# Optimization experiments

Measured on AMD Instinct MI355X. Metric: run time of the kernel, lower is better.

The kernel has to match this reference:

```python
import jax, jax.numpy as jnp
import numpy as np

B, N, D = 64, 128, 32
P = N * (N - 1)          # ordered pairs
H1, H2, HF = 32, 32, 16  # layer_widths=(32,32), final_widths=(16,)
EPS = 1e-5
SLOPE = 0.01             # LeakyReLU default


def _leaky(x):
    return jnp.where(x >= 0, x, SLOPE * x)


def setup_inputs() -> dict:
    key = jax.random.key(0)
    ks = jax.random.split(key, 16)
    # all ordered pairs (i, j), i != j, grouped by source i
    src = np.repeat(np.arange(N), N - 1)
    tgt = np.array([j for i in range(N) for j in range(N) if j != i])
    s = 0.1
    return {
        "inputs": jax.random.normal(ks[0], (B, N, D), jnp.float32),
        "src": jnp.asarray(src, jnp.int32),
        "tgt": jnp.asarray(tgt, jnp.int32),
        # edge MLP: Linear(2D,32) -> BN1d(P) -> LeakyReLU -> Linear(32,32) -> LeakyReLU -> Linear(32, 1+D)
        "W1": jax.random.normal(ks[1], (2 * D, H1), jnp.float32) * s,
        "b1": jnp.zeros((H1,), jnp.float32),
        "g1": jnp.ones((P,), jnp.float32),
        "be1": jnp.zeros((P,), jnp.float32),
        "W2": jax.random.normal(ks[2], (H1, H2), jnp.float32) * s,
        "b2": jnp.zeros((H2,), jnp.float32),
        "W3": jax.random.normal(ks[3], (H2, 1 + D), jnp.float32) * s,
        "b3": jnp.zeros((1 + D,), jnp.float32),
        # final MLP: Linear(2D,16) -> BN1d(16) -> LeakyReLU -> Linear(16, D)
        "Wf1": jax.random.normal(ks[4], (2 * D, HF), jnp.float32) * s,
        "bf1": jnp.zeros((HF,), jnp.float32),
        "gf": jnp.ones((HF,), jnp.float32),
        "bef": jnp.zeros((HF,), jnp.float32),
        "Wf2": jax.random.normal(ks[5], (HF, D), jnp.float32) * s,
        "bf2": jnp.zeros((D,), jnp.float32),
    }


def reference(inputs, src, tgt, W1, b1, g1, be1, W2, b2, W3, b3,
              Wf1, bf1, gf, bef, Wf2, bf2):
    b, n, d = inputs.shape
    # gather pair features: (B, P, 2D)
    paired = jnp.concatenate([inputs[:, src], inputs[:, tgt]], axis=2)
    h = paired @ W1 + b1                              # (B, P, H1)
    # BatchNorm1d(P) on (B, P, H1): normalize per pair channel over (batch, feat)
    m = h.mean(axis=(0, 2), keepdims=True)
    v = h.var(axis=(0, 2), keepdims=True)
    h = (h - m) * jax.lax.rsqrt(v + EPS) * g1[None, :, None] + be1[None, :, None]
    h = _leaky(h) @ W2 + b2
    h = _leaky(h) @ W3 + b3                           # (B, P, 1+D)
    edges = jax.nn.sigmoid(h[..., :1])                # (B, P, 1)
    messages = h[..., 1:]                             # (B, P, D)
    weighted = edges * messages
    # segment-sum over the (N-1) senders per source node
    agg = weighted.reshape(b, n, n - 1, d).sum(axis=2)  # (B, N, D)
    sm = jnp.concatenate([inputs, agg], axis=2).reshape(-1, 2 * d)
    f = sm @ Wf1 + bf1                                # (B*N, HF)
    mf = f.mean(axis=0)
    vf = f.var(axis=0)
    f = (f - mf) * jax.lax.rsqrt(vf + EPS) * gf + bef
    out = _leaky(f) @ Wf2 + bf2
    return edges[..., 0], out.reshape(b, n, d)
```

## Files before the change

### kernel.cpp

```cpp
#include <hip/hip_runtime.h>
#include <hip/hip_bf16.h>
#include <math.h>

#define BB 64
#define NN 128
#define DD 32
#define PP (NN * (NN - 1))
#define EPSF 1e-5f

typedef __attribute__((ext_vector_type(8))) short bf16x8;
typedef __attribute__((ext_vector_type(4))) float f32x4;

static __device__ __forceinline__ unsigned short f2bf(float x) {
    unsigned u = __builtin_bit_cast(unsigned, x);
    u += 0x7fff + ((u >> 16) & 1);
    return (unsigned short)(u >> 16);
}
static __device__ __forceinline__ unsigned pk2bf(float a, float b) {
    float2 t; t.x = a; t.y = b;
    __hip_bfloat162 h = __float22bfloat162_rn(t);
    unsigned u;
    __builtin_memcpy(&u, &h, 4);
    return u;
}
static __device__ __forceinline__ float leakyf(float x) {
    return fmaxf(x, 0.01f * x);
}

__global__ __launch_bounds__(256) void proj_kernel(
    const float* __restrict__ inputs, const float* __restrict__ W1,
    const float* __restrict__ b1,
    const float* __restrict__ W2, const float* __restrict__ W3,
    float* __restrict__ AT, float* __restrict__ BT,
    unsigned short* __restrict__ ATh, unsigned short* __restrict__ BTh,
    float* __restrict__ SQp,
    unsigned short* __restrict__ W2p, unsigned short* __restrict__ W3p,
    float* __restrict__ fpartA, float* __restrict__ fpartB)
{
    __shared__ float Xs[16 * 33];
    __shared__ float W1s[2048];
    __shared__ float red[16];

    int tid = threadIdx.x;
    int n = blockIdx.x >> 2, q = blockIdx.x & 3;

    for (int idx = tid; idx < 2048; idx += 256) W1s[idx] = W1[idx];
    for (int idx = tid; idx < 512; idx += 256) {
        int r = idx >> 5, d = idx & 31;
        Xs[r * 33 + d] = inputs[(size_t)(q * 16 + r) * 4096 + n * 32 + d];
    }
    __syncthreads();

    int j = tid & 31, rb = tid >> 5;
    int lane = tid & 63, w = tid >> 6;
    float b1j = b1[j];
    float sa = 0.f, qa = 0.f, sb = 0.f, qb = 0.f;
    #pragma unroll
    for (int i = 0; i < 2; ++i) {
        int r = rb * 2 + i;
        int b = q * 16 + r;
        float a = b1j, c = 0.f;
        #pragma unroll
        for (int k = 0; k < 32; ++k) {
            float x = Xs[r * 33 + k];
            a += x * W1s[k * 32 + j];
            c += x * W1s[(32 + k) * 32 + j];
        }
        size_t off = ((size_t)n * 64 + b) * 32 + j;
        AT[off] = a;  BT[off] = c;
        ATh[off] = f2bf(a);  BTh[off] = f2bf(c);
        sa += a; qa += a * a; sb += c; qb += c * c;
    }
    #pragma unroll
    for (int d = 32; d > 0; d >>= 1) {
        sa += __shfl_down(sa, d, 64);
        qa += __shfl_down(qa, d, 64);
        sb += __shfl_down(sb, d, 64);
        qb += __shfl_down(qb, d, 64);
    }
    if (lane == 0) { red[w*4+0] = sa; red[w*4+1] = qa; red[w*4+2] = sb; red[w*4+3] = qb; }
    __syncthreads();
    if (tid == 0) {
        float4 v;
        v.x = red[0] + red[4] + red[8]  + red[12];
        v.y = red[1] + red[5] + red[9]  + red[13];
        v.z = red[2] + red[6] + red[10] + red[14];
        v.w = red[3] + red[7] + red[11] + red[15];
        ((float4*)SQp)[n * 4 + q] = v;
    }

    if (blockIdx.x == 0 && tid < 64) {
        int l = tid, nn2 = l & 15, kc = l >> 4;
        #pragma unroll
        for (int ct = 0; ct < 2; ++ct)
            #pragma unroll
            for (int jj = 0; jj < 8; ++jj) {
                int k = kc * 8 + jj;
                W2p[(ct * 64 + l) * 8 + jj] = f2bf(W2[k * 32 + ct * 16 + nn2]);
            }
        #pragma unroll
        for (int ct = 0; ct < 3; ++ct)
            #pragma unroll
            for (int jj = 0; jj < 8; ++jj) {
                int k = kc * 8 + jj;
                int c2 = ct * 16 + nn2;
                W3p[(ct * 64 + l) * 8 + jj] = f2bf(c2 < 33 ? W3[k * 33 + c2] : 0.f);
            }
    }
    if (blockIdx.x == 1) {
        for (int idx = tid; idx < 1024; idx += 256) {
            fpartA[idx] = 0.f;
            fpartB[idx] = 0.f;
        }
    }
}

__global__ __launch_bounds__(256) void stats2_kernel(
    const unsigned short* __restrict__ ATh, const unsigned short* __restrict__ BTh,
    const float* __restrict__ SQp,
    const float* __restrict__ g1, const float* __restrict__ be1,
    float* __restrict__ statA, float* __restrict__ statB)
{
    __shared__ __align__(16) float part[4 * 64 * 4];
    int tid = threadIdx.x;
    int lane = tid & 63, w = tid >> 6;
    int s0 = (blockIdx.x >> 3) * 16, t0 = (blockIdx.x & 7) * 16;

    int m = lane & 15, kc = lane >> 4;
    const unsigned short* abase = ATh + (size_t)(s0 + m) * 2048 + kc * 8 + w * 512;
    const unsigned short* bbase = BTh + (size_t)(t0 + m) * 2048 + kc * 8 + w * 512;

    f32x4 acc0 = {0.f, 0.f, 0.f, 0.f}, acc1 = {0.f, 0.f, 0.f, 0.f};
    #pragma unroll
    for (int step = 0; step < 8; ++step) {
        bf16x8 av0 = *(const bf16x8*)(abase + (2 * step) * 32);
        bf16x8 bv0 = *(const bf16x8*)(bbase + (2 * step) * 32);
        acc0 = __builtin_amdgcn_mfma_f32_16x16x32_bf16(av0, bv0, acc0, 0, 0, 0);
        bf16x8 av1 = *(const bf16x8*)(abase + (2 * step + 1) * 32);
        bf16x8 bv1 = *(const bf16x8*)(bbase + (2 * step + 1) * 32);
        acc1 = __builtin_amdgcn_mfma_f32_16x16x32_bf16(av1, bv1, acc1, 0, 0, 0);
    }
    f32x4 acc;
    acc[0] = acc0[0] + acc1[0]; acc[1] = acc0[1] + acc1[1];
    acc[2] = acc0[2] + acc1[2]; acc[3] = acc0[3] + acc1[3];
    *(f32x4*)&part[(w * 64 + lane) * 4] = acc;
    __syncthreads();

    if (w == 0) {
        #pragma unroll
        for (int ww = 1; ww < 4; ++ww) {
            f32x4 o2 = *(const f32x4*)&part[(ww * 64 + lane) * 4];
            acc[0] += o2[0]; acc[1] += o2[1]; acc[2] += o2[2]; acc[3] += o2[3];
        }
        int col = lane & 15, quad = lane >> 4;
        int t = t0 + col;
        float sbt = 0.f, qbt = 0.f;
        #pragma unroll
        for (int o2 = 0; o2 < 4; ++o2) {
            float4 v = ((const float4*)SQp)[t * 4 + o2];
            sbt += v.z; qbt += v.w;
        }
        #pragma unroll
        for (int r = 0; r < 4; ++r) {
            int s = s0 + quad * 4 + r;
            if (s != t) {
                float sas = 0.f, qas = 0.f;
                #pragma unroll
                for (int o2 = 0; o2 < 4; ++o2) {
                    float4 v = ((const float4*)SQp)[s * 4 + o2];
                    sas += v.x; qas += v.y;
                }
                int e = t - (t > s);
                int p = s * 127 + e;
                float S = sas + sbt;
                float Q = qas + qbt + 2.f * acc[r];
                float mean = S * (1.f / 2048.f);
                float var  = Q * (1.f / 2048.f) - mean * mean;
                float inv  = rsqrtf(var + EPSF);
                float sc   = inv * g1[p];
                statA[p] = sc;
                statB[p] = be1[p] - mean * sc;
            }
        }
    }
}

__global__ __launch_bounds__(256) void edges_kernel(
    const float* __restrict__ AT, const float* __restrict__ BT,
    const float* __restrict__ statA, const float* __restrict__ statB,
    const unsigned short* __restrict__ W2p, const unsigned short* __restrict__ W3p,
    const float* __restrict__ b2, const float* __restrict__ b3,
    const float* __restrict__ inputs, const float* __restrict__ Wf1,
    const float* __restrict__ bf1,
    float* __restrict__ edges_out,
    float* __restrict__ f, float* __restrict__ fpartA, float* __restrict__ fpartB)
{
    __shared__ __align__(16) unsigned short Hs[4][512];
    __shared__ float Wf1s[1024];
    __shared__ float aggbuf[4][32];

    int tid = threadIdx.x;
    int s = blockIdx.x & 127;
    int b = blockIdx.x >> 7;
    int lane = tid & 63, w = tid >> 6;
    int m = lane & 15;
    int kb = lane >> 4;
    int col = m;
    int q4 = kb * 4;
    int qbase = lane & 48;

    for (int idx = tid; idx < 1024; idx += 256) Wf1s[idx] = Wf1[idx];

    bf16x8 wb2[2], wb3[3];
    wb2[0] = *(const bf16x8*)(W2p + (0 * 64 + lane) * 8);
    wb2[1] = *(const bf16x8*)(W2p + (1 * 64 + lane) * 8);
    wb3[0] = *(const bf16x8*)(W3p + (0 * 64 + lane) * 8);
    wb3[1] = *(const bf16x8*)(W3p + (1 * 64 + lane) * 8);
    wb3[2] = *(const bf16x8*)(W3p + (2 * 64 + lane) * 8);
    float b2c0 = b2[col], b2c1 = b2[16 + col];
    float b3c[3];
    #pragma unroll
    for (int ct = 0; ct < 3; ++ct) {
        int c = ct * 16 + col;
        b3c[ct] = (c < 33) ? b3[c] : 0.f;
    }

    const float4* asl = (const float4*)(AT + ((size_t)s * 64 + b) * 32 + kb * 8);
    float4 a0 = asl[0], a1 = asl[1];

    float aggpart[3] = {0.f, 0.f, 0.f};

    #pragma unroll
    for (int rt = 0; rt < 2; ++rt) {
        int tile = w * 2 + rt;
        int e = tile * 16 + m;
        bool valid = (e < 127);
        int ee = valid ? e : 0;
        int t = ee + (ee >= s);
        int p = s * 127 + ee;
        float sc = statA[p], sh = statB[p];

        const float4* bsl = (const float4*)(BT + ((size_t)t * 64 + b) * 32 + kb * 8);
        float4 bv0 = bsl[0], bv1 = bsl[1];

        float nh[8];
        nh[0] = leakyf((a0.x + bv0.x) * sc + sh);
        nh[1] = leakyf((a0.y + bv0.y) * sc + sh);
        nh[2] = leakyf((a0.z + bv0.z) * sc + sh);
        nh[3] = leakyf((a0.w + bv0.w) * sc + sh);
        nh[4] = leakyf((a1.x + bv1.x) * sc + sh);
        nh[5] = leakyf((a1.y + bv1.y) * sc + sh);
        nh[6] = leakyf((a1.z + bv1.z) * sc + sh);
        nh[7] = leakyf((a1.w + bv1.w) * sc + sh);
        if (!valid) {
            #pragma unroll
            for (int q = 0; q < 8; ++q) nh[q] = 0.f;
        }
        union { bf16x8 v; unsigned u[4]; } AF;
        #pragma unroll
        for (int q = 0; q < 4; ++q) AF.u[q] = pk2bf(nh[2*q], nh[2*q+1]);

        f32x4 c0 = {0.f, 0.f, 0.f, 0.f}, c1 = {0.f, 0.f, 0.f, 0.f};
        c0 = __builtin_amdgcn_mfma_f32_16x16x32_bf16(AF.v, wb2[0], c0, 0, 0, 0);
        c1 = __builtin_amdgcn_mfma_f32_16x16x32_bf16(AF.v, wb2[1], c1, 0, 0, 0);

        #pragma unroll
        for (int reg = 0; reg < 4; ++reg) {
            int row = q4 + reg;
            float x = leakyf(c0[reg] + b2c0);
            float y = leakyf(c1[reg] + b2c1);
            int cA = col;
            int cB = col + 16;
            Hs[w][row * 32 + (((cA >> 3) ^ (row >> 2)) & 3) * 8 + (cA & 7)] = f2bf(x);
            Hs[w][row * 32 + (((cB >> 3) ^ (row >> 2)) & 3) * 8 + (cB & 7)] = f2bf(y);
        }
        bf16x8 a2 = *(const bf16x8*)&Hs[w][m * 32 + ((kb ^ (m >> 2)) & 3) * 8];

        f32x4 oo[3];
        #pragma unroll
        for (int ct = 0; ct < 3; ++ct) {
            f32x4 cc = {0.f, 0.f, 0.f, 0.f};
            oo[ct] = __builtin_amdgcn_mfma_f32_16x16x32_bf16(a2, wb3[ct], cc, 0, 0, 0);
        }

        float v0 = 0.f, v1 = 0.f, v2 = 0.f, v3 = 0.f;
        int grow0 = tile * 16 + q4;
        if (col == 0) {
            v0 = 1.f / (1.f + __expf(-(oo[0][0] + b3c[0])));
            v1 = 1.f / (1.f + __expf(-(oo[0][1] + b3c[0])));
            v2 = 1.f / (1.f + __expf(-(oo[0][2] + b3c[0])));
            v3 = (grow0 == 124) ? 0.f
               : 1.f / (1.f + __expf(-(oo[0][3] + b3c[0])));
            float* ep = edges_out + (size_t)b * PP + s * 127 + grow0;
            ep[0] = v0; ep[1] = v1; ep[2] = v2;
            if (grow0 != 124) ep[3] = v3;
        }
        float ev0 = __shfl(v0, qbase, 64);
        float ev1 = __shfl(v1, qbase, 64);
        float ev2 = __shfl(v2, qbase, 64);
        float ev3 = __shfl(v3, qbase, 64);

        #pragma unroll
        for (int ct = 0; ct < 3; ++ct) {
            float bb3 = b3c[ct];
            float pt = ev0 * (oo[ct][0] + bb3) + ev1 * (oo[ct][1] + bb3)
                     + ev2 * (oo[ct][2] + bb3) + ev3 * (oo[ct][3] + bb3);
            aggpart[ct] += pt;
        }
    }

    #pragma unroll
    for (int ct = 0; ct < 3; ++ct) {
        float pt = aggpart[ct];
        pt += __shfl_xor(pt, 16, 64);
        pt += __shfl_xor(pt, 32, 64);
        int c = ct * 16 + col;
        if (kb == 0 && c >= 1 && c <= 32) aggbuf[w][c - 1] = pt;
    }
    __syncthreads();

    if (tid < 16) {
        size_t row = (size_t)b * 128 + s;
        const float* xrow = inputs + row * 32;
        float acc = bf1[tid];
        #pragma unroll
        for (int k = 0; k < 32; ++k) acc += xrow[k] * Wf1s[k * 16 + tid];
        #pragma unroll
        for (int k = 0; k < 32; ++k) {
            float tot = aggbuf[0][k] + aggbuf[1][k] + aggbuf[2][k] + aggbuf[3][k];
            acc += tot * Wf1s[(32 + k) * 16 + tid];
        }
        f[row * 16 + tid] = acc;
        int bucket = blockIdx.x & 63;
        atomicAdd(&fpartA[bucket * 16 + tid], acc);
        atomicAdd(&fpartB[bucket * 16 + tid], acc * acc);
    }
}

__global__ __launch_bounds__(256) void out_kernel(
    const float* __restrict__ f,
    const float* __restrict__ fpartA, const float* __restrict__ fpartB,
    const float* __restrict__ gf, const float* __restrict__ bef,
    const float* __restrict__ Wf2, const float* __restrict__ bf2,
    float* __restrict__ outp)
{
    __shared__ float Wf2s[512];
    __shared__ float sc[16], sh[16];
    __shared__ float fs[128];

    int tid = threadIdx.x;
    for (int idx = tid; idx < 512; idx += 256) Wf2s[idx] = Wf2[idx];
    if (tid < 16) {
        float S = 0.f, Q = 0.f;
        #pragma unroll
        for (int g = 0; g < 64; ++g) {
            S += fpartA[g * 16 + tid];
            Q += fpartB[g * 16 + tid];
        }
        float mean = S * (1.f / 8192.f);
        float var  = Q * (1.f / 8192.f) - mean * mean;
        float inv  = rsqrtf(var + EPSF);
        float s2   = inv * gf[tid];
        sc[tid] = s2;
        sh[tid] = bef[tid] - mean * s2;
    }
    int row0 = blockIdx.x * 8;
    if (tid < 128) {
        int r = tid >> 4, j = tid & 15;
        fs[r * 16 + j] = f[(size_t)(row0 + r) * 16 + j];
    }
    __syncthreads();

    int rl = tid >> 5, d = tid & 31;
    float acc = bf2[d];
    #pragma unroll
    for (int j = 0; j < 16; ++j) {
        float v = fs[rl * 16 + j] * sc[j] + sh[j];
        v = leakyf(v);
        acc += v * Wf2s[j * 32 + d];
    }
    outp[(size_t)(row0 + rl) * 32 + d] = acc;
}

extern "C" void kernel_launch(void* const* d_in, const int* in_sizes, int n_in,
                              void* d_out, int out_size, void* d_ws, size_t ws_size,
                              hipStream_t stream) {
    const float* inputs = (const float*)d_in[0];
    const float* W1   = (const float*)d_in[3];
    const float* b1   = (const float*)d_in[4];
    const float* g1   = (const float*)d_in[5];
    const float* be1  = (const float*)d_in[6];
    const float* W2   = (const float*)d_in[7];
    const float* b2   = (const float*)d_in[8];
    const float* W3   = (const float*)d_in[9];
    const float* b3   = (const float*)d_in[10];
    const float* Wf1  = (const float*)d_in[11];
    const float* bf1  = (const float*)d_in[12];
    const float* gf   = (const float*)d_in[13];
    const float* bef  = (const float*)d_in[14];
    const float* Wf2  = (const float*)d_in[15];
    const float* bf2  = (const float*)d_in[16];

    float* ws = (float*)d_ws;
    float* AT     = ws;
    float* BT     = ws + 262144;
    unsigned short* ATh = (unsigned short*)(ws + 524288);
    unsigned short* BTh = ATh + 262144;
    float* SQp    = ws + 786432;
    float* statA  = ws + 790528;
    float* statB  = ws + 806784;
    float* f      = ws + 823040;
    float* fpartA = ws + 954112;
    float* fpartB = ws + 955136;
    unsigned short* W2p = (unsigned short*)(ws + 956160);
    unsigned short* W3p = W2p + 1024;

    float* edges_out = (float*)d_out;
    float* outp      = edges_out + (size_t)BB * PP;

    proj_kernel<<<512, 256, 0, stream>>>(inputs, W1, b1, W2, W3,
                                         AT, BT, ATh, BTh, SQp,
                                         W2p, W3p, fpartA, fpartB);
    stats2_kernel<<<64, 256, 0, stream>>>(ATh, BTh, SQp, g1, be1, statA, statB);
    edges_kernel<<<8192, 256, 0, stream>>>(AT, BT, statA, statB, W2p, W3p,
                                           b2, b3, inputs, Wf1, bf1,
                                           edges_out, f, fpartA, fpartB);
    out_kernel<<<1024, 256, 0, stream>>>(f, fpartA, fpartB, gf, bef, Wf2, bf2, outp);
}
```

Measured before the change: 144.2 us.

## Fuse four kernels into one persistent kernel with software grid barriers

Merges the projection, pair-statistics, edge MLP and output kernels into a single 1024-block persistent kernel. Atomic-counter grid barriers separate the phases, and the edge phase loops over multiple (batch, source) work items per block. This removes three kernel launch gaps and tail effects, at the cost of spin-wait barriers that need every block co-resident, plus an extra memset launch. Occupancy is capped by a launch bound of 4 blocks per SM.

```diff
diff --git a/kernel.cpp b/kernel.cpp
--- a/kernel.cpp
+++ b/kernel.cpp
@@ -7,6 +7,7 @@
 #define DD 32
 #define PP (NN * (NN - 1))
 #define EPSF 1e-5f
+#define GRID 1024
 
 typedef __attribute__((ext_vector_type(8))) short bf16x8;
 typedef __attribute__((ext_vector_type(4))) float f32x4;
@@ -27,359 +28,368 @@
     return fmaxf(x, 0.01f * x);
 }
 
-__global__ __launch_bounds__(256) void proj_kernel(
+static __device__ __forceinline__ void grid_sync(unsigned* cnt) {
+    __syncthreads();
+    if (threadIdx.x == 0) {
+        __hip_atomic_fetch_add(cnt, 1u, __ATOMIC_ACQ_REL, __HIP_MEMORY_SCOPE_AGENT);
+        while (__hip_atomic_load(cnt, __ATOMIC_ACQUIRE, __HIP_MEMORY_SCOPE_AGENT)
+               < (unsigned)GRID)
+            __builtin_amdgcn_s_sleep(8);
+    }
+    __syncthreads();
+}
+
+__global__ __launch_bounds__(256, 4) void fused_kernel(
     const float* __restrict__ inputs, const float* __restrict__ W1,
-    const float* __restrict__ b1,
-    const float* __restrict__ W2, const float* __restrict__ W3,
+    const float* __restrict__ b1, const float* __restrict__ g1,
+    const float* __restrict__ be1, const float* __restrict__ W2,
+    const float* __restrict__ b2, const float* __restrict__ W3,
+    const float* __restrict__ b3, const float* __restrict__ Wf1,
+    const float* __restrict__ bf1, const float* __restrict__ gf,
+    const float* __restrict__ bef, const float* __restrict__ Wf2,
+    const float* __restrict__ bf2,
     float* __restrict__ AT, float* __restrict__ BT,
     unsigned short* __restrict__ ATh, unsigned short* __restrict__ BTh,
-    float* __restrict__ SQp,
+    float* __restrict__ SQp, float* __restrict__ statA, float* __restrict__ statB,
+    float* __restrict__ f, float* __restrict__ fpartA, float* __restrict__ fpartB,
     unsigned short* __restrict__ W2p, unsigned short* __restrict__ W3p,
-    float* __restrict__ fpartA, float* __restrict__ fpartB)
+    float* __restrict__ edges_out, float* __restrict__ outp,
+    unsigned* __restrict__ cnt)
 {
-    __shared__ float Xs[16 * 33];
-    __shared__ float W1s[2048];
-    __shared__ float red[16];
-
+    __shared__ __align__(16) char smem[10368];
     int tid = threadIdx.x;
-    int n = blockIdx.x >> 2, q = blockIdx.x & 3;
-
-    for (int idx = tid; idx < 2048; idx += 256) W1s[idx] = W1[idx];
-    for (int idx = tid; idx < 512; idx += 256) {
-        int r = idx >> 5, d = idx & 31;
-        Xs[r * 33 + d] = inputs[(size_t)(q * 16 + r) * 4096 + n * 32 + d];
-    }
-    __syncthreads();
-
-    int j = tid & 31, rb = tid >> 5;
+    int bx = blockIdx.x;
     int lane = tid & 63, w = tid >> 6;
-    float b1j = b1[j];
-    float sa = 0.f, qa = 0.f, sb = 0.f, qb = 0.f;
-    #pragma unroll
-    for (int i = 0; i < 2; ++i) {
-        int r = rb * 2 + i;
-        int b = q * 16 + r;
-        float a = b1j, c = 0.f;
+
+    if (bx < 512) {
+        float* Xs  = (float*)smem;
+        float* W1s = (float*)smem + 528;
+        float* red = (float*)smem + 2576;
+        int n = bx >> 2, q = bx & 3;
+
+        for (int idx = tid; idx < 2048; idx += 256) W1s[idx] = W1[idx];
+        for (int idx = tid; idx < 512; idx += 256) {
+            int r = idx >> 5, d = idx & 31;
+            Xs[r * 33 + d] = inputs[(size_t)(q * 16 + r) * 4096 + n * 32 + d];
+        }
+        __syncthreads();
+
+        int j = tid & 31, rb = tid >> 5;
+        float b1j = b1[j];
+        float sa = 0.f, qa = 0.f, sb = 0.f, qb = 0.f;
         #pragma unroll
-        for (int k = 0; k < 32; ++k) {
-            float x = Xs[r * 33 + k];
-            a += x * W1s[k * 32 + j];
-            c += x * W1s[(32 + k) * 32 + j];
-        }
-        size_t off = ((size_t)n * 64 + b) * 32 + j;
-        AT[off] = a;  BT[off] = c;
-        ATh[off] = f2bf(a);  BTh[off] = f2bf(c);
-        sa += a; qa += a * a; sb += c; qb += c * c;
-    }
-    #pragma unroll
-    for (int d = 32; d > 0; d >>= 1) {
-        sa += __shfl_down(sa, d, 64);
-        qa += __shfl_down(qa, d, 64);
-        sb += __shfl_down(sb, d, 64);
-        qb += __shfl_down(qb, d, 64);
-    }
-    if (lane == 0) { red[w*4+0] = sa; red[w*4+1] = qa; red[w*4+2] = sb; red[w*4+3] = qb; }
-    __syncthreads();
-    if (tid == 0) {
-        float4 v;
-        v.x = red[0] + red[4] + red[8]  + red[12];
-        v.y = red[1] + red[5] + red[9]  + red[13];
-        v.z = red[2] + red[6] + red[10] + red[14];
-        v.w = red[3] + red[7] + red[11] + red[15];
-        ((float4*)SQp)[n * 4 + q] = v;
-    }
-
-    if (blockIdx.x == 0 && tid < 64) {
-        int l = tid, nn2 = l & 15, kc = l >> 4;
+        for (int i = 0; i < 2; ++i) {
+            int r = rb * 2 + i;
+            int b = q * 16 + r;
+            float a = b1j, c = 0.f;
+            #pragma unroll
+            for (int k = 0; k < 32; ++k) {
+                float x = Xs[r * 33 + k];
+                a += x * W1s[k * 32 + j];
+                c += x * W1s[(32 + k) * 32 + j];
+            }
+            size_t off = ((size_t)n * 64 + b) * 32 + j;
+            AT[off] = a;  BT[off] = c;
+            ATh[off] = f2bf(a);  BTh[off] = f2bf(c);
+            sa += a; qa += a * a; sb += c; qb += c * c;
+        }
         #pragma unroll
-        for (int ct = 0; ct < 2; ++ct)
-            #pragma unroll
-            for (int jj = 0; jj < 8; ++jj) {
-                int k = kc * 8 + jj;
-                W2p[(ct * 64 + l) * 8 + jj] = f2bf(W2[k * 32 + ct * 16 + nn2]);
-            }
-        #pragma unroll
-        for (int ct = 0; ct < 3; ++ct)
-            #pragma unroll
-            for (int jj = 0; jj < 8; ++jj) {
-                int k = kc * 8 + jj;
-                int c2 = ct * 16 + nn2;
-                W3p[(ct * 64 + l) * 8 + jj] = f2bf(c2 < 33 ? W3[k * 33 + c2] : 0.f);
-            }
-    }
-    if (blockIdx.x == 1) {
+        for (int d = 32; d > 0; d >>= 1) {
+            sa += __shfl_down(sa, d, 64);
+            qa += __shfl_down(qa, d, 64);
+            sb += __shfl_down(sb, d, 64);
+            qb += __shfl_down(qb, d, 64);
+        }
+        if (lane == 0) { red[w*4+0] = sa; red[w*4+1] = qa; red[w*4+2] = sb; red[w*4+3] = qb; }
+        __syncthreads();
+        if (tid == 0) {
+            float4 v;
+            v.x = red[0] + red[4] + red[8]  + red[12];
+            v.y = red[1] + red[5] + red[9]  + red[13];
+            v.z = red[2] + red[6] + red[10] + red[14];
+            v.w = red[3] + red[7] + red[11] + red[15];
+            ((float4*)SQp)[n * 4 + q] = v;
+        }
+    } else if (bx == 512) {
+        if (tid < 64) {
+            int l = tid, nn2 = l & 15, kc = l >> 4;
+            #pragma unroll
+            for (int ct = 0; ct < 2; ++ct)
+                #pragma unroll
+                for (int jj = 0; jj < 8; ++jj) {
+                    int k = kc * 8 + jj;
+                    W2p[(ct * 64 + l) * 8 + jj] = f2bf(W2[k * 32 + ct * 16 + nn2]);
+                }
+            #pragma unroll
+            for (int ct = 0; ct < 3; ++ct)
+                #pragma unroll
+                for (int jj = 0; jj < 8; ++jj) {
+                    int k = kc * 8 + jj;
+                    int c2 = ct * 16 + nn2;
+                    W3p[(ct * 64 + l) * 8 + jj] = f2bf(c2 < 33 ? W3[k * 33 + c2] : 0.f);
+                }
+        }
+    } else if (bx == 513) {
         for (int idx = tid; idx < 1024; idx += 256) {
             fpartA[idx] = 0.f;
             fpartB[idx] = 0.f;
         }
     }
-}
-
-__global__ __launch_bounds__(256) void stats2_kernel(
-    const unsigned short* __restrict__ ATh, const unsigned short* __restrict__ BTh,
-    const float* __restrict__ SQp,
-    const float* __restrict__ g1, const float* __restrict__ be1,
-    float* __restrict__ statA, float* __restrict__ statB)
-{
-    __shared__ __align__(16) float part[4 * 64 * 4];
-    int tid = threadIdx.x;
-    int lane = tid & 63, w = tid >> 6;
-    int s0 = (blockIdx.x >> 3) * 16, t0 = (blockIdx.x & 7) * 16;
-
-    int m = lane & 15, kc = lane >> 4;
-    const unsigned short* abase = ATh + (size_t)(s0 + m) * 2048 + kc * 8 + w * 512;
-    const unsigned short* bbase = BTh + (size_t)(t0 + m) * 2048 + kc * 8 + w * 512;
-
-    f32x4 acc0 = {0.f, 0.f, 0.f, 0.f}, acc1 = {0.f, 0.f, 0.f, 0.f};
-    #pragma unroll
-    for (int step = 0; step < 8; ++step) {
-        bf16x8 av0 = *(const bf16x8*)(abase + (2 * step) * 32);
-        bf16x8 bv0 = *(const bf16x8*)(bbase + (2 * step) * 32);
-        acc0 = __builtin_amdgcn_mfma_f32_16x16x32_bf16(av0, bv0, acc0, 0, 0, 0);
-        bf16x8 av1 = *(const bf16x8*)(abase + (2 * step + 1) * 32);
-        bf16x8 bv1 = *(const bf16x8*)(bbase + (2 * step + 1) * 32);
-        acc1 = __builtin_amdgcn_mfma_f32_16x16x32_bf16(av1, bv1, acc1, 0, 0, 0);
+
+    grid_sync(cnt + 0);
+
+    if (bx < 64) {
+        float* part = (float*)smem;
+        int s0 = (bx >> 3) * 16, t0 = (bx & 7) * 16;
+        int m = lane & 15, kc = lane >> 4;
+        const unsigned short* abase = ATh + (size_t)(s0 + m) * 2048 + kc * 8 + w * 512;
+        const unsigned short* bbase = BTh + (size_t)(t0 + m) * 2048 + kc * 8 + w * 512;
+
+        f32x4 acc0 = {0.f, 0.f, 0.f, 0.f}, acc1 = {0.f, 0.f, 0.f, 0.f};
+        #pragma unroll
+        for (int step = 0; step < 8; ++step) {
+            bf16x8 av0 = *(const bf16x8*)(abase + (2 * step) * 32);
+            bf16x8 bv0 = *(const bf16x8*)(bbase + (2 * step) * 32);
+            acc0 = __builtin_amdgcn_mfma_f32_16x16x32_bf16(av0, bv0, acc0, 0, 0, 0);
+            bf16x8 av1 = *(const bf16x8*)(abase + (2 * step + 1) * 32);
+            bf16x8 bv1 = *(const bf16x8*)(bbase + (2 * step + 1) * 32);
+            acc1 = __builtin_amdgcn_mfma_f32_16x16x32_bf16(av1, bv1, acc1, 0, 0, 0);
+        }
+        f32x4 acc;
+        acc[0] = acc0[0] + acc1[0]; acc[1] = acc0[1] + acc1[1];
+        acc[2] = acc0[2] + acc1[2]; acc[3] = acc0[3] + acc1[3];
+        *(f32x4*)&part[(w * 64 + lane) * 4] = acc;
+        __syncthreads();
+
+        if (w == 0) {
+            #pragma unroll
+            for (int ww = 1; ww < 4; ++ww) {
+                f32x4 o2 = *(const f32x4*)&part[(ww * 64 + lane) * 4];
+                acc[0] += o2[0]; acc[1] += o2[1]; acc[2] += o2[2]; acc[3] += o2[3];
+            }
+            int col = lane & 15, quad = lane >> 4;
+            int t = t0 + col;
+            float sbt = 0.f, qbt = 0.f;
+            #pragma unroll
+            for (int o2 = 0; o2 < 4; ++o2) {
+                float4 v = ((const float4*)SQp)[t * 4 + o2];
+                sbt += v.z; qbt += v.w;
+            }
+            #pragma unroll
+            for (int r = 0; r < 4; ++r) {
+                int s = s0 + quad * 4 + r;
+                if (s != t) {
+                    float sas = 0.f, qas = 0.f;
+                    #pragma unroll
+                    for (int o2 = 0; o2 < 4; ++o2) {
+                        float4 v = ((const float4*)SQp)[s * 4 + o2];
+                        sas += v.x; qas += v.y;
+                    }
+                    int e = t - (t > s);
+                    int p = s * 127 + e;
+                    float S = sas + sbt;
+                    float Q = qas + qbt + 2.f * acc[r];
+                    float mean = S * (1.f / 2048.f);
+                    float var  = Q * (1.f / 2048.f) - mean * mean;
+                    float inv  = rsqrtf(var + EPSF);
+                    float sc   = inv * g1[p];
+                    statA[p] = sc;
+                    statB[p] = be1[p] - mean * sc;
+                }
+            }
+        }
     }
-    f32x4 acc;
-    acc[0] = acc0[0] + acc1[0]; acc[1] = acc0[1] + acc1[1];
-    acc[2] = acc0[2] + acc1[2]; acc[3] = acc0[3] + acc1[3];
-    *(f32x4*)&part[(w * 64 + lane) * 4] = acc;
-    __syncthreads();
-
-    if (w == 0) {
-        #pragma unroll
-        for (int ww = 1; ww < 4; ++ww) {
-            f32x4 o2 = *(const f32x4*)&part[(ww * 64 + lane) * 4];
-            acc[0] += o2[0]; acc[1] += o2[1]; acc[2] += o2[2]; acc[3] += o2[3];
-        }
-        int col = lane & 15, quad = lane >> 4;
-        int t = t0 + col;
-        float sbt = 0.f, qbt = 0.f;
-        #pragma unroll
-        for (int o2 = 0; o2 < 4; ++o2) {
-            float4 v = ((const float4*)SQp)[t * 4 + o2];
-            sbt += v.z; qbt += v.w;
-        }
-        #pragma unroll
-        for (int r = 0; r < 4; ++r) {
-            int s = s0 + quad * 4 + r;
-            if (s != t) {
-                float sas = 0.f, qas = 0.f;
-                #pragma unroll
-                for (int o2 = 0; o2 < 4; ++o2) {
-                    float4 v = ((const float4*)SQp)[s * 4 + o2];
-                    sas += v.x; qas += v.y;
-                }
-                int e = t - (t > s);
-                int p = s * 127 + e;
-                float S = sas + sbt;
-                float Q = qas + qbt + 2.f * acc[r];
-                float mean = S * (1.f / 2048.f);
-                float var  = Q * (1.f / 2048.f) - mean * mean;
-                float inv  = rsqrtf(var + EPSF);
-                float sc   = inv * g1[p];
-                statA[p] = sc;
-                statB[p] = be1[p] - mean * sc;
-            }
-        }
-    }
-}
-
-__global__ __launch_bounds__(256) void edges_kernel(
-    const float* __restrict__ AT, const float* __restrict__ BT,
-    const float* __restrict__ statA, const float* __restrict__ statB,
-    const unsigned short* __restrict__ W2p, const unsigned short* __restrict__ W3p,
-    const float* __restrict__ b2, const float* __restrict__ b3,
-    const float* __restrict__ inputs, const float* __restrict__ Wf1,
-    const float* __restrict__ bf1,
-    float* __restrict__ edges_out,
-    float* __restrict__ f, float* __restrict__ fpartA, float* __restrict__ fpartB)
-{
-    __shared__ __align__(16) unsigned short Hs[4][512];
-    __shared__ float Wf1s[1024];
-    __shared__ float aggbuf[4][32];
-
-    int tid = threadIdx.x;
-    int s = blockIdx.x & 127;
-    int b = blockIdx.x >> 7;
-    int lane = tid & 63, w = tid >> 6;
-    int m = lane & 15;
-    int kb = lane >> 4;
-    int col = m;
-    int q4 = kb * 4;
-    int qbase = lane & 48;
-
-    for (int idx = tid; idx < 1024; idx += 256) Wf1s[idx] = Wf1[idx];
-
-    bf16x8 wb2[2], wb3[3];
-    wb2[0] = *(const bf16x8*)(W2p + (0 * 64 + lane) * 8);
-    wb2[1] = *(const bf16x8*)(W2p + (1 * 64 + lane) * 8);
-    wb3[0] = *(const bf16x8*)(W3p + (0 * 64 + lane) * 8);
-    wb3[1] = *(const bf16x8*)(W3p + (1 * 64 + lane) * 8);
-    wb3[2] = *(const bf16x8*)(W3p + (2 * 64 + lane) * 8);
-    float b2c0 = b2[col], b2c1 = b2[16 + col];
-    float b3c[3];
-    #pragma unroll
-    for (int ct = 0; ct < 3; ++ct) {
-        int c = ct * 16 + col;
-        b3c[ct] = (c < 33) ? b3[c] : 0.f;
-    }
-
-    const float4* asl = (const float4*)(AT + ((size_t)s * 64 + b) * 32 + kb * 8);
-    float4 a0 = asl[0], a1 = asl[1];
-
-    float aggpart[3] = {0.f, 0.f, 0.f};
-
-    #pragma unroll
-    for (int rt = 0; rt < 2; ++rt) {
-        int tile = w * 2 + rt;
-        int e = tile * 16 + m;
-        bool valid = (e < 127);
-        int ee = valid ? e : 0;
-        int t = ee + (ee >= s);
-        int p = s * 127 + ee;
-        float sc = statA[p], sh = statB[p];
-
-        const float4* bsl = (const float4*)(BT + ((size_t)t * 64 + b) * 32 + kb * 8);
-        float4 bv0 = bsl[0], bv1 = bsl[1];
-
-        float nh[8];
-        nh[0] = leakyf((a0.x + bv0.x) * sc + sh);
-        nh[1] = leakyf((a0.y + bv0.y) * sc + sh);
-        nh[2] = leakyf((a0.z + bv0.z) * sc + sh);
-        nh[3] = leakyf((a0.w + bv0.w) * sc + sh);
-        nh[4] = leakyf((a1.x + bv1.x) * sc + sh);
-        nh[5] = leakyf((a1.y + bv1.y) * sc + sh);
-        nh[6] = leakyf((a1.z + bv1.z) * sc + sh);
-        nh[7] = leakyf((a1.w + bv1.w) * sc + sh);
-        if (!valid) {
-            #pragma unroll
-            for (int q = 0; q < 8; ++q) nh[q] = 0.f;
-        }
-        union { bf16x8 v; unsigned u[4]; } AF;
-        #pragma unroll
-        for (int q = 0; q < 4; ++q) AF.u[q] = pk2bf(nh[2*q], nh[2*q+1]);
-
-        f32x4 c0 = {0.f, 0.f, 0.f, 0.f}, c1 = {0.f, 0.f, 0.f, 0.f};
-        c0 = __builtin_amdgcn_mfma_f32_16x16x32_bf16(AF.v, wb2[0], c0, 0, 0, 0);
-        c1 = __builtin_amdgcn_mfma_f32_16x16x32_bf16(AF.v, wb2[1], c1, 0, 0, 0);
-
-        #pragma unroll
-        for (int reg = 0; reg < 4; ++reg) {
-            int row = q4 + reg;
-            float x = leakyf(c0[reg] + b2c0);
-            float y = leakyf(c1[reg] + b2c1);
-            int cA = col;
-            int cB = col + 16;
-            Hs[w][row * 32 + (((cA >> 3) ^ (row >> 2)) & 3) * 8 + (cA & 7)] = f2bf(x);
-            Hs[w][row * 32 + (((cB >> 3) ^ (row >> 2)) & 3) * 8 + (cB & 7)] = f2bf(y);
-        }
-        bf16x8 a2 = *(const bf16x8*)&Hs[w][m * 32 + ((kb ^ (m >> 2)) & 3) * 8];
-
-        f32x4 oo[3];
+
+    grid_sync(cnt + 1);
+
+    {
+        unsigned short (*Hs)[512] = (unsigned short (*)[512])smem;
+        float* Wf1s = (float*)(smem + 4096);
+        float (*aggbuf)[4][32] = (float (*)[4][32])(smem + 8192);
+
+        int m = lane & 15;
+        int kb = lane >> 4;
+        int col = m;
+        int q4 = kb * 4;
+        int qbase = lane & 48;
+
+        for (int idx = tid; idx < 1024; idx += 256) Wf1s[idx] = Wf1[idx];
+
+        bf16x8 wb2[2], wb3[3];
+        wb2[0] = *(const bf16x8*)(W2p + (0 * 64 + lane) * 8);
+        wb2[1] = *(const bf16x8*)(W2p + (1 * 64 + lane) * 8);
+        wb3[0] = *(const bf16x8*)(W3p + (0 * 64 + lane) * 8);
+        wb3[1] = *(const bf16x8*)(W3p + (1 * 64 + lane) * 8);
+        wb3[2] = *(const bf16x8*)(W3p + (2 * 64 + lane) * 8);
+        float b2c0 = b2[col], b2c1 = b2[16 + col];
+        float b3c[3];
         #pragma unroll
         for (int ct = 0; ct < 3; ++ct) {
-            f32x4 cc = {0.f, 0.f, 0.f, 0.f};
-            oo[ct] = __builtin_amdgcn_mfma_f32_16x16x32_bf16(a2, wb3[ct], cc, 0, 0, 0);
-        }
-
-        float v0 = 0.f, v1 = 0.f, v2 = 0.f, v3 = 0.f;
-        int grow0 = tile * 16 + q4;
-        if (col == 0) {
-            v0 = 1.f / (1.f + __expf(-(oo[0][0] + b3c[0])));
-            v1 = 1.f / (1.f + __expf(-(oo[0][1] + b3c[0])));
-            v2 = 1.f / (1.f + __expf(-(oo[0][2] + b3c[0])));
-            v3 = (grow0 == 124) ? 0.f
-               : 1.f / (1.f + __expf(-(oo[0][3] + b3c[0])));
-            float* ep = edges_out + (size_t)b * PP + s * 127 + grow0;
-            ep[0] = v0; ep[1] = v1; ep[2] = v2;
-            if (grow0 != 124) ep[3] = v3;
-        }
-        float ev0 = __shfl(v0, qbase, 64);
-        float ev1 = __shfl(v1, qbase, 64);
-        float ev2 = __shfl(v2, qbase, 64);
-        float ev3 = __shfl(v3, qbase, 64);
-
+            int c = ct * 16 + col;
+            b3c[ct] = (c < 33) ? b3[c] : 0.f;
+        }
+
+        int bb2 = bx >> 4;
+        int sbase = (bx & 15) * 8;
+
+        for (int vi = 0; vi < 8; ++vi) {
+            int s = sbase + vi;
+            const float4* asl = (const float4*)(AT + ((size_t)s * 64 + bb2) * 32 + kb * 8);
+            float4 a0 = asl[0], a1 = asl[1];
+
+            float aggpart[3] = {0.f, 0.f, 0.f};
+
+            #pragma unroll
+            for (int rt = 0; rt < 2; ++rt) {
+                int tile = w * 2 + rt;
+                int e = tile * 16 + m;
+                bool valid = (e < 127);
+                int ee = valid ? e : 0;
+                int t = ee + (ee >= s);
+                int p = s * 127 + ee;
+                float sc = statA[p], sh = statB[p];
+
+                const float4* bsl = (const float4*)(BT + ((size_t)t * 64 + bb2) * 32 + kb * 8);
+                float4 bv0 = bsl[0], bv1 = bsl[1];
+
+                float nh[8];
+                nh[0] = leakyf((a0.x + bv0.x) * sc + sh);
+                nh[1] = leakyf((a0.y + bv0.y) * sc + sh);
+                nh[2] = leakyf((a0.z + bv0.z) * sc + sh);
+                nh[3] = leakyf((a0.w + bv0.w) * sc + sh);
+                nh[4] = leakyf((a1.x + bv1.x) * sc + sh);
+                nh[5] = leakyf((a1.y + bv1.y) * sc + sh);
+                nh[6] = leakyf((a1.z + bv1.z) * sc + sh);
+                nh[7] = leakyf((a1.w + bv1.w) * sc + sh);
+                if (!valid) {
+                    #pragma unroll
+                    for (int q = 0; q < 8; ++q) nh[q] = 0.f;
+                }
+                union { bf16x8 v; unsigned u[4]; } AF;
+                #pragma unroll
+                for (int q = 0; q < 4; ++q) AF.u[q] = pk2bf(nh[2*q], nh[2*q+1]);
+
+                f32x4 c0 = {0.f, 0.f, 0.f, 0.f}, c1 = {0.f, 0.f, 0.f, 0.f};
+                c0 = __builtin_amdgcn_mfma_f32_16x16x32_bf16(AF.v, wb2[0], c0, 0, 0, 0);
+                c1 = __builtin_amdgcn_mfma_f32_16x16x32_bf16(AF.v, wb2[1], c1, 0, 0, 0);
+
+                #pragma unroll
+                for (int reg = 0; reg < 4; ++reg) {
+                    int row = q4 + reg;
+                    float x = leakyf(c0[reg] + b2c0);
+                    float y = leakyf(c1[reg] + b2c1);
+                    int cA = col;
+                    int cB = col + 16;
+                    Hs[w][row * 32 + (((cA >> 3) ^ (row >> 2)) & 3) * 8 + (cA & 7)] = f2bf(x);
+                    Hs[w][row * 32 + (((cB >> 3) ^ (row >> 2)) & 3) * 8 + (cB & 7)] = f2bf(y);
+                }
+                bf16x8 a2 = *(const bf16x8*)&Hs[w][m * 32 + ((kb ^ (m >> 2)) & 3) * 8];
+
+                f32x4 oo[3];
+                #pragma unroll
+                for (int ct = 0; ct < 3; ++ct) {
+                    f32x4 cc = {0.f, 0.f, 0.f, 0.f};
+                    oo[ct] = __builtin_amdgcn_mfma_f32_16x16x32_bf16(a2, wb3[ct], cc, 0, 0, 0);
+                }
+
+                float v0 = 0.f, v1 = 0.f, v2 = 0.f, v3 = 0.f;
+                int grow0 = tile * 16 + q4;
+                if (col == 0) {
+                    v0 = 1.f / (1.f + __expf(-(oo[0][0] + b3c[0])));
+                    v1 = 1.f / (1.f + __expf(-(oo[0][1] + b3c[0])));
+                    v2 = 1.f / (1.f + __expf(-(oo[0][2] + b3c[0])));
+                    v3 = (grow0 == 124) ? 0.f
+                       : 1.f / (1.f + __expf(-(oo[0][3] + b3c[0])));
+                    float* ep = edges_out + (size_t)bb2 * PP + s * 127 + grow0;
+                    ep[0] = v0; ep[1] = v1; ep[2] = v2;
+                    if (grow0 != 124) ep[3] = v3;
+                }
+                float ev0 = __shfl(v0, qbase, 64);
+                float ev1 = __shfl(v1, qbase, 64);
+                float ev2 = __shfl(v2, qbase, 64);
+                float ev3 = __shfl(v3, qbase, 64);
+
+                #pragma unroll
+                for (int ct = 0; ct < 3; ++ct) {
+                    float bb3 = b3c[ct];
+                    float pt = ev0 * (oo[ct][0] + bb3) + ev1 * (oo[ct][1] + bb3)
+                             + ev2 * (oo[ct][2] + bb3) + ev3 * (oo[ct][3] + bb3);
+                    aggpart[ct] += pt;
+                }
+            }
+
+            int par = vi & 1;
+            #pragma unroll
+            for (int ct = 0; ct < 3; ++ct) {
+                float pt = aggpart[ct];
+                pt += __shfl_xor(pt, 16, 64);
+                pt += __shfl_xor(pt, 32, 64);
+                int c = ct * 16 + col;
+                if (kb == 0 && c >= 1 && c <= 32) aggbuf[par][w][c - 1] = pt;
+            }
+            __syncthreads();
+
+            if (w == (vi & 3) && lane < 16) {
+                int j = lane;
+                size_t row = (size_t)bb2 * 128 + s;
+                const float* xrow = inputs + row * 32;
+                float acc = bf1[j];
+                #pragma unroll
+                for (int k = 0; k < 32; ++k) acc += xrow[k] * Wf1s[k * 16 + j];
+                #pragma unroll
+                for (int k = 0; k < 32; ++k) {
+                    float tot = aggbuf[par][0][k] + aggbuf[par][1][k]
+                              + aggbuf[par][2][k] + aggbuf[par][3][k];
+                    acc += tot * Wf1s[(32 + k) * 16 + j];
+                }
+                f[row * 16 + j] = acc;
+                int bucket = s & 63;
+                atomicAdd(&fpartA[bucket * 16 + j], acc);
+                atomicAdd(&fpartB[bucket * 16 + j], acc * acc);
+            }
+        }
+    }
+
+    grid_sync(cnt + 2);
+
+    {
+        float* Wf2s = (float*)smem;
+        float* scv  = (float*)smem + 512;
+        float* shv  = (float*)smem + 528;
+        float* fs   = (float*)smem + 544;
+
+        for (int idx = tid; idx < 512; idx += 256) Wf2s[idx] = Wf2[idx];
+        if (tid < 16) {
+            float S = 0.f, Q = 0.f;
+            #pragma unroll
+            for (int g = 0; g < 64; ++g) {
+                S += fpartA[g * 16 + tid];
+                Q += fpartB[g * 16 + tid];
+            }
+            float mean = S * (1.f / 8192.f);
+            float var  = Q * (1.f / 8192.f) - mean * mean;
+            float inv  = rsqrtf(var + EPSF);
+            float s2   = inv * gf[tid];
+            scv[tid] = s2;
+            shv[tid] = bef[tid] - mean * s2;
+        }
+        int row0 = bx * 8;
+        if (tid < 128) {
+            int r = tid >> 4, j = tid & 15;
+            fs[r * 16 + j] = f[(size_t)(row0 + r) * 16 + j];
+        }
+        __syncthreads();
+
+        int rl = tid >> 5, d = tid & 31;
+        float acc = bf2[d];
         #pragma unroll
-        for (int ct = 0; ct < 3; ++ct) {
-            float bb3 = b3c[ct];
-            float pt = ev0 * (oo[ct][0] + bb3) + ev1 * (oo[ct][1] + bb3)
-                     + ev2 * (oo[ct][2] + bb3) + ev3 * (oo[ct][3] + bb3);
-            aggpart[ct] += pt;
-        }
+        for (int j2 = 0; j2 < 16; ++j2) {
+            float v = fs[rl * 16 + j2] * scv[j2] + shv[j2];
+            v = leakyf(v);
+            acc += v * Wf2s[j2 * 32 + d];
+        }
+        outp[(size_t)(row0 + rl) * 32 + d] = acc;
     }
-
-    #pragma unroll
-    for (int ct = 0; ct < 3; ++ct) {
-        float pt = aggpart[ct];
-        pt += __shfl_xor(pt, 16, 64);
-        pt += __shfl_xor(pt, 32, 64);
-        int c = ct * 16 + col;
-        if (kb == 0 && c >= 1 && c <= 32) aggbuf[w][c - 1] = pt;
-    }
-    __syncthreads();
-
-    if (tid < 16) {
-        size_t row = (size_t)b * 128 + s;
-        const float* xrow = inputs + row * 32;
-        float acc = bf1[tid];
-        #pragma unroll
-        for (int k = 0; k < 32; ++k) acc += xrow[k] * Wf1s[k * 16 + tid];
-        #pragma unroll
-        for (int k = 0; k < 32; ++k) {
-            float tot = aggbuf[0][k] + aggbuf[1][k] + aggbuf[2][k] + aggbuf[3][k];
-            acc += tot * Wf1s[(32 + k) * 16 + tid];
-        }
-        f[row * 16 + tid] = acc;
-        int bucket = blockIdx.x & 63;
-        atomicAdd(&fpartA[bucket * 16 + tid], acc);
-        atomicAdd(&fpartB[bucket * 16 + tid], acc * acc);
-    }
-}
-
-__global__ __launch_bounds__(256) void out_kernel(
-    const float* __restrict__ f,
-    const float* __restrict__ fpartA, const float* __restrict__ fpartB,
-    const float* __restrict__ gf, const float* __restrict__ bef,
-    const float* __restrict__ Wf2, const float* __restrict__ bf2,
-    float* __restrict__ outp)
-{
-    __shared__ float Wf2s[512];
-    __shared__ float sc[16], sh[16];
-    __shared__ float fs[128];
-
-    int tid = threadIdx.x;
-    for (int idx = tid; idx < 512; idx += 256) Wf2s[idx] = Wf2[idx];
-    if (tid < 16) {
-        float S = 0.f, Q = 0.f;
-        #pragma unroll
-        for (int g = 0; g < 64; ++g) {
-            S += fpartA[g * 16 + tid];
-            Q += fpartB[g * 16 + tid];
-        }
-        float mean = S * (1.f / 8192.f);
-        float var  = Q * (1.f / 8192.f) - mean * mean;
-        float inv  = rsqrtf(var + EPSF);
-        float s2   = inv * gf[tid];
-        sc[tid] = s2;
-        sh[tid] = bef[tid] - mean * s2;
-    }
-    int row0 = blockIdx.x * 8;
-    if (tid < 128) {
-        int r = tid >> 4, j = tid & 15;
-        fs[r * 16 + j] = f[(size_t)(row0 + r) * 16 + j];
-    }
-    __syncthreads();
-
-    int rl = tid >> 5, d = tid & 31;
-    float acc = bf2[d];
-    #pragma unroll
-    for (int j = 0; j < 16; ++j) {
-        float v = fs[rl * 16 + j] * sc[j] + sh[j];
-        v = leakyf(v);
-        acc += v * Wf2s[j * 32 + d];
-    }
-    outp[(size_t)(row0 + rl) * 32 + d] = acc;
 }
 
 extern "C" void kernel_launch(void* const* d_in, const int* in_sizes, int n_in,
@@ -414,16 +424,14 @@
     float* fpartB = ws + 955136;
     unsigned short* W2p = (unsigned short*)(ws + 956160);
     unsigned short* W3p = W2p + 1024;
+    unsigned* cnt = (unsigned*)(ws + 788480);
 
     float* edges_out = (float*)d_out;
     float* outp      = edges_out + (size_t)BB * PP;
 
-    proj_kernel<<<512, 256, 0, stream>>>(inputs, W1, b1, W2, W3,
-                                         AT, BT, ATh, BTh, SQp,
-                                         W2p, W3p, fpartA, fpartB);
-    stats2_kernel<<<64, 256, 0, stream>>>(ATh, BTh, SQp, g1, be1, statA, statB);
-    edges_kernel<<<8192, 256, 0, stream>>>(AT, BT, statA, statB, W2p, W3p,
-                                           b2, b3, inputs, Wf1, bf1,
-                                           edges_out, f, fpartA, fpartB);
-    out_kernel<<<1024, 256, 0, stream>>>(f, fpartA, fpartB, gf, bef, Wf2, bf2, outp);
-}
+    hipMemsetAsync(cnt, 0, 16, stream);
+    fused_kernel<<<GRID, 256, 0, stream>>>(
+        inputs, W1, b1, g1, be1, W2, b2, W3, b3, Wf1, bf1, gf, bef, Wf2, bf2,
+        AT, BT, ATh, BTh, SQp, statA, statB, f, fpartA, fpartB, W2p, W3p,
+        edges_out, outp, cnt);
+}
```

Measured after the change: 440.3 us. 205% more time.
